# Kernel tuning notes

Measured on AMD Instinct MI355X. Metric: run time of the kernel, lower is better.

Reference implementation:

```python
import jax, jax.numpy as jnp
import numpy as np


def setup_inputs() -> dict:
    key = jax.random.key(0)
    k1, k2 = jax.random.split(key)
    B, C, H, W, D = 4, 32, 256, 512, 48
    h1 = jax.random.normal(k1, (B, C, H, W), dtype=jnp.float32)
    cost = jax.random.normal(k2, (B, D, H, W), dtype=jnp.float32)
    return {"h1": h1, "cost": cost}


def reference(h1, cost):
    # g2[b,c,h,w] = sum_d cost[b,d,h,w] * stop_grad(h1)[b,c,h,w+d]  for w+d < W
    # (original torch code detaches h1, so grads only flow through cost)
    B, C, H, W = h1.shape
    D = cost.shape[1]
    h1d = jax.lax.stop_gradient(h1)
    w_idx = jnp.arange(W)

    # scan over disparity levels; each step does a masked roll + fused MAC,
    # never materializing the [B,C,D,H,W] shifted stack.
    cost_d_major = jnp.moveaxis(cost, 1, 0)  # [D,B,H,W]

    def step(acc, xd):
        d, c_d = xd  # c_d: [B,H,W]
        valid = (w_idx < (W - d)).astype(h1.dtype)  # [W]; zero beyond W-d
        shifted = jnp.roll(h1d, -d, axis=-1) * valid  # h1[..., w+d], zero-padded
        acc = acc + c_d[:, None, :, :] * shifted  # broadcast over C
        return acc, None

    g2, _ = jax.lax.scan(step, jnp.zeros_like(h1), (jnp.arange(D), cost_d_major))
    return g2
```

## Files before the change

### kernel.cpp

```cpp
#include <hip/hip_runtime.h>


#define BB 4
#define CC 32
#define CHB 16
#define HH 256
#define WW 512
#define DDISP 48
#define HW (HH * WW)
#define TW 256
#define WROW 312
#define NT 512

__global__ __launch_bounds__(NT, 4)
void dense_warp_kernel(const float* __restrict__ h1,
                       const float* __restrict__ cost,
                       float* __restrict__ out)
{
    __shared__ float h1s[CHB * WROW];

    const int blk    = blockIdx.x;
    const int wside  = blk & 1;
    const int h      = (blk >> 1) & (HH - 1);
    const int chalf  = (blk >> 9) & 1;
    const int b      = blk >> 10;
    const int wstart = wside * TW;
    const int tid    = threadIdx.x;

    {
        const float* src = h1 + (((size_t)b * CC + chalf * CHB) * HH + (size_t)h) * WW;
        for (int idx = tid; idx < CHB * 78; idx += NT) {
            int r    = idx / 78;
            int q    = idx - r * 78;
            int col  = q << 2;
            int wsrc = wstart + col;
            float4 v = make_float4(0.f, 0.f, 0.f, 0.f);
            if (wsrc < WW) v = *(const float4*)(src + (size_t)r * HW + wsrc);
            *(float4*)(&h1s[r * WROW + col]) = v;
        }
    }
    __syncthreads();

    const int lane = tid & 63;
    const int wid  = tid >> 6;
    const int c0   = wid << 1;
    const int w0   = lane << 2;

    float acc[2][4];
#pragma unroll
    for (int c = 0; c < 2; ++c)
#pragma unroll
        for (int j = 0; j < 4; ++j) acc[c][j] = 0.f;

    float win[2][8];
    const float* lptr = &h1s[c0 * WROW + w0];
#pragma unroll
    for (int c = 0; c < 2; ++c) {
        float4 q0 = *(const float4*)(lptr + c * WROW);
        float4 q1 = *(const float4*)(lptr + c * WROW + 4);
        win[c][0] = q0.x; win[c][1] = q0.y; win[c][2] = q0.z; win[c][3] = q0.w;
        win[c][4] = q1.x; win[c][5] = q1.y; win[c][6] = q1.z; win[c][7] = q1.w;
    }

    const float* cp = cost + ((size_t)b * DDISP * HH + (size_t)h) * WW + wstart + w0;

    float cv[4][4];

#pragma unroll
    for (int g = 0; g < 12; ++g) {
        const int P = g & 1;
#pragma unroll
        for (int dd = 0; dd < 4; ++dd) {
            float4 t = *(const float4*)(cp + (size_t)(4 * g + dd) * HW);
            cv[dd][0] = t.x; cv[dd][1] = t.y; cv[dd][2] = t.z; cv[dd][3] = t.w;
        }
#pragma unroll
        for (int c = 0; c < 2; ++c) {
#pragma unroll
            for (int dd = 0; dd < 4; ++dd)
#pragma unroll
                for (int j = 0; j < 4; ++j) {
                    const int o    = dd + j;
                    const int slot = (P + (o >> 2)) & 1;
                    acc[c][j] += cv[dd][j] * win[c][slot * 4 + (o & 3)];
                }
            float4 t = *(const float4*)(lptr + c * WROW + 8);
            win[c][P * 4 + 0] = t.x; win[c][P * 4 + 1] = t.y;
            win[c][P * 4 + 2] = t.z; win[c][P * 4 + 3] = t.w;
        }
        lptr += 4;
    }

    float* outBase = out + (((size_t)b * CC + chalf * CHB) * HH + (size_t)h) * WW
                     + wstart + w0;
#pragma unroll
    for (int c = 0; c < 2; ++c) {
        float* op = outBase + (size_t)(c0 + c) * HW;
        *(float4*)op = make_float4(acc[c][0], acc[c][1], acc[c][2], acc[c][3]);
    }
}

extern "C" void kernel_launch(void* const* d_in, const int* in_sizes, int n_in,
                              void* d_out, int out_size, void* d_ws, size_t ws_size,
                              hipStream_t stream) {
    const float* h1   = (const float*)d_in[0];
    const float* cost = (const float*)d_in[1];
    float* out        = (float*)d_out;
    dim3 grid(BB * HH * 2 * 2);
    dense_warp_kernel<<<grid, NT, 0, stream>>>(h1, cost, out);
}
```

Measured before the change: 248.7 us.

## Drop shared-memory staging and read h1 windows directly from global memory

Removes the LDS tile and barrier. Each thread now loads its sliding h1 window straight from global memory with clamped float4 loads, masking the out-of-range tail to zero. Blocks shrink to 256 threads covering 8 channels, and the grid doubles to 4 channel groups. As a result each cost row is re-read by 4 blocks instead of 2, which adds cost traffic, largely served by L2. The intent is to cut staging latency and the sync while raising block count and occupancy.

```diff
diff --git a/kernel.cpp b/kernel.cpp
--- a/kernel.cpp
+++ b/kernel.cpp
@@ -3,101 +3,81 @@
 
 #define BB 4
 #define CC 32
-#define CHB 16
 #define HH 256
 #define WW 512
 #define DDISP 48
 #define HW (HH * WW)
 #define TW 256
-#define WROW 312
-#define NT 512
+#define NT 256
+
+__device__ __forceinline__ void ldh(const float* __restrict__ row, int wq,
+                                    float* __restrict__ dst)
+{
+    int wc = wq > (WW - 4) ? (WW - 4) : wq;
+    float4 t = *(const float4*)(row + wc);
+    bool ok = wq < WW;
+    dst[0] = ok ? t.x : 0.f;
+    dst[1] = ok ? t.y : 0.f;
+    dst[2] = ok ? t.z : 0.f;
+    dst[3] = ok ? t.w : 0.f;
+}
 
 __global__ __launch_bounds__(NT, 4)
 void dense_warp_kernel(const float* __restrict__ h1,
                        const float* __restrict__ cost,
                        float* __restrict__ out)
 {
-    __shared__ float h1s[CHB * WROW];
-
     const int blk    = blockIdx.x;
     const int wside  = blk & 1;
     const int h      = (blk >> 1) & (HH - 1);
-    const int chalf  = (blk >> 9) & 1;
-    const int b      = blk >> 10;
+    const int cgrp   = (blk >> 9) & 3;
+    const int b      = blk >> 11;
     const int wstart = wside * TW;
-    const int tid    = threadIdx.x;
 
-    {
-        const float* src = h1 + (((size_t)b * CC + chalf * CHB) * HH + (size_t)h) * WW;
-        for (int idx = tid; idx < CHB * 78; idx += NT) {
-            int r    = idx / 78;
-            int q    = idx - r * 78;
-            int col  = q << 2;
-            int wsrc = wstart + col;
-            float4 v = make_float4(0.f, 0.f, 0.f, 0.f);
-            if (wsrc < WW) v = *(const float4*)(src + (size_t)r * HW + wsrc);
-            *(float4*)(&h1s[r * WROW + col]) = v;
-        }
-    }
-    __syncthreads();
+    const int lane = threadIdx.x & 63;
+    const int wid  = threadIdx.x >> 6;
+    const int c0   = (cgrp << 3) + (wid << 1);
+    const int w0   = lane << 2;
+    const int wq0  = wstart + w0;
 
-    const int lane = tid & 63;
-    const int wid  = tid >> 6;
-    const int c0   = wid << 1;
-    const int w0   = lane << 2;
+    const float* r0 = h1 + (((size_t)b * CC + c0    ) * HH + h) * WW;
+    const float* r1 = h1 + (((size_t)b * CC + c0 + 1) * HH + h) * WW;
 
-    float acc[2][4];
-#pragma unroll
-    for (int c = 0; c < 2; ++c)
-#pragma unroll
-        for (int j = 0; j < 4; ++j) acc[c][j] = 0.f;
+    float acc0[4] = {0.f, 0.f, 0.f, 0.f};
+    float acc1[4] = {0.f, 0.f, 0.f, 0.f};
 
-    float win[2][8];
-    const float* lptr = &h1s[c0 * WROW + w0];
-#pragma unroll
-    for (int c = 0; c < 2; ++c) {
-        float4 q0 = *(const float4*)(lptr + c * WROW);
-        float4 q1 = *(const float4*)(lptr + c * WROW + 4);
-        win[c][0] = q0.x; win[c][1] = q0.y; win[c][2] = q0.z; win[c][3] = q0.w;
-        win[c][4] = q1.x; win[c][5] = q1.y; win[c][6] = q1.z; win[c][7] = q1.w;
-    }
+    float win0[8], win1[8];
+    ldh(r0, wq0,     &win0[0]);  ldh(r0, wq0 + 4, &win0[4]);
+    ldh(r1, wq0,     &win1[0]);  ldh(r1, wq0 + 4, &win1[4]);
 
-    const float* cp = cost + ((size_t)b * DDISP * HH + (size_t)h) * WW + wstart + w0;
-
-    float cv[4][4];
+    const float* cp = cost + ((size_t)b * DDISP * HH + h) * WW + wq0;
 
 #pragma unroll
     for (int g = 0; g < 12; ++g) {
         const int P = g & 1;
+        float cv[4][4];
 #pragma unroll
         for (int dd = 0; dd < 4; ++dd) {
             float4 t = *(const float4*)(cp + (size_t)(4 * g + dd) * HW);
             cv[dd][0] = t.x; cv[dd][1] = t.y; cv[dd][2] = t.z; cv[dd][3] = t.w;
         }
 #pragma unroll
-        for (int c = 0; c < 2; ++c) {
+        for (int dd = 0; dd < 4; ++dd)
 #pragma unroll
-            for (int dd = 0; dd < 4; ++dd)
-#pragma unroll
-                for (int j = 0; j < 4; ++j) {
-                    const int o    = dd + j;
-                    const int slot = (P + (o >> 2)) & 1;
-                    acc[c][j] += cv[dd][j] * win[c][slot * 4 + (o & 3)];
-                }
-            float4 t = *(const float4*)(lptr + c * WROW + 8);
-            win[c][P * 4 + 0] = t.x; win[c][P * 4 + 1] = t.y;
-            win[c][P * 4 + 2] = t.z; win[c][P * 4 + 3] = t.w;
-        }
-        lptr += 4;
+            for (int j = 0; j < 4; ++j) {
+                const int o    = dd + j;
+                const int slot = (P + (o >> 2)) & 1;
+                acc0[j] += cv[dd][j] * win0[slot * 4 + (o & 3)];
+                acc1[j] += cv[dd][j] * win1[slot * 4 + (o & 3)];
+            }
+        ldh(r0, wq0 + 4 * g + 8, &win0[P * 4]);
+        ldh(r1, wq0 + 4 * g + 8, &win1[P * 4]);
     }
 
-    float* outBase = out + (((size_t)b * CC + chalf * CHB) * HH + (size_t)h) * WW
-                     + wstart + w0;
-#pragma unroll
-    for (int c = 0; c < 2; ++c) {
-        float* op = outBase + (size_t)(c0 + c) * HW;
-        *(float4*)op = make_float4(acc[c][0], acc[c][1], acc[c][2], acc[c][3]);
-    }
+    float* o0 = out + (((size_t)b * CC + c0    ) * HH + h) * WW + wq0;
+    float* o1 = out + (((size_t)b * CC + c0 + 1) * HH + h) * WW + wq0;
+    *(float4*)o0 = make_float4(acc0[0], acc0[1], acc0[2], acc0[3]);
+    *(float4*)o1 = make_float4(acc1[0], acc1[1], acc1[2], acc1[3]);
 }
 
 extern "C" void kernel_launch(void* const* d_in, const int* in_sizes, int n_in,
@@ -106,6 +86,6 @@
     const float* h1   = (const float*)d_in[0];
     const float* cost = (const float*)d_in[1];
     float* out        = (float*)d_out;
-    dim3 grid(BB * HH * 2 * 2);
+    dim3 grid(BB * HH * 2 * 4);
     dense_warp_kernel<<<grid, NT, 0, stream>>>(h1, cost, out);
 }
```

Result: slower. 282.4 us (+13.6%).
